# Kernel tuning notes

Measured on AMD Instinct MI355X. Metric: run time of the kernel, lower is better.

## Reference

```python
import jax, jax.numpy as jnp
import numpy as np

SIZE = 1024
CODE_DIM = 256
N = 65536

def setup_inputs() -> dict:
    key = jax.random.key(0)
    k1, k2 = jax.random.split(key)
    z = jax.random.normal(k1, (N, CODE_DIM), dtype=jnp.float32)
    # nn.Embedding weight initialized uniform(-1/size, 1/size)
    weight = jax.random.uniform(k2, (SIZE, CODE_DIM), dtype=jnp.float32,
                                minval=-1.0 / SIZE, maxval=1.0 / SIZE)
    return {"z": z, "weight": weight}

def reference(z, weight):
    flat = z.reshape(-1, CODE_DIM)                       # [N, D]
    distances = (jnp.sum(flat ** 2, axis=1, keepdims=True)
                 - 2.0 * flat @ weight.T
                 + jnp.sum(weight ** 2, axis=1)[None, :])  # [N, SIZE]
    encoding_indices = jnp.argmax(-distances, axis=1)     # [N]
    quantized = weight[encoding_indices]                  # [N, D]
    return quantized, encoding_indices
```

## Files before the change

### kernel.cpp

```cpp
#include <hip/hip_runtime.h>
#include <hip/hip_bf16.h>
#include <stdint.h>
#include <float.h>


constexpr int NROWS = 65536;
constexpr int D     = 256;
constexpr int CODES = 1024;

constexpr float TAU_SCREEN = 2.5e-4f;
constexpr int   MAXPAIRS   = 7000000;

typedef __attribute__((ext_vector_type(8))) short short8;
typedef __attribute__((ext_vector_type(4))) float f32x4;

__device__ __forceinline__ void gl2lds16(const unsigned short* g, unsigned short* l) {
    __builtin_amdgcn_global_load_lds(
        (const __attribute__((address_space(1))) void*)g,
        (__attribute__((address_space(3))) void*)l, 16, 0, 0);
}

__device__ __forceinline__ unsigned short f2bf(float x) {
    union { __hip_bfloat16 h; unsigned short u; } c;
    c.h = __float2bfloat16(x);
    return c.u;
}

__device__ __forceinline__ uint4 pack8(float4 a, float4 b) {
    union { unsigned short u[8]; uint4 v; } p;
    p.u[0] = f2bf(a.x); p.u[1] = f2bf(a.y); p.u[2] = f2bf(a.z); p.u[3] = f2bf(a.w);
    p.u[4] = f2bf(b.x); p.u[5] = f2bf(b.y); p.u[6] = f2bf(b.z); p.u[7] = f2bf(b.w);
    return p.v;
}

__device__ __forceinline__ void cvt8(const float* __restrict__ src,
                                     unsigned short* __restrict__ dst, int i) {
    const float4* s = (const float4*)src + (size_t)i * 2;
    *(uint4*)(dst + (size_t)i * 8) = pack8(s[0], s[1]);
}

__global__ __launch_bounds__(256) void vq_prep(const float* __restrict__ w,
                                               unsigned short* __restrict__ wbf,
                                               float* __restrict__ Cn,
                                               int* __restrict__ cnt,
                                               int* __restrict__ pcnt,
                                               unsigned long long* __restrict__ packed) {
    const int b = blockIdx.x;
    const int t = threadIdx.x;
    if (b < 128) {
        cvt8(w, wbf, b * 256 + t);
    } else if (b < 132) {
        const int row = (b - 128) * 256 + t;
        const float4* p = (const float4*)(w + (size_t)row * D);
        float res[2];
        #pragma unroll
        for (int h = 0; h < 2; ++h) {
            float r[8];
            #pragma unroll
            for (int j = 0; j < 8; ++j) r[j] = 0.f;
            #pragma unroll 4
            for (int mm = 0; mm < 16; ++mm) {
                const float4 v0 = p[h * 32 + mm * 2];
                const float4 v1 = p[h * 32 + mm * 2 + 1];
                r[0] = __fadd_rn(r[0], __fmul_rn(v0.x, v0.x));
                r[1] = __fadd_rn(r[1], __fmul_rn(v0.y, v0.y));
                r[2] = __fadd_rn(r[2], __fmul_rn(v0.z, v0.z));
                r[3] = __fadd_rn(r[3], __fmul_rn(v0.w, v0.w));
                r[4] = __fadd_rn(r[4], __fmul_rn(v1.x, v1.x));
                r[5] = __fadd_rn(r[5], __fmul_rn(v1.y, v1.y));
                r[6] = __fadd_rn(r[6], __fmul_rn(v1.z, v1.z));
                r[7] = __fadd_rn(r[7], __fmul_rn(v1.w, v1.w));
            }
            res[h] = __fadd_rn(__fadd_rn(__fadd_rn(r[0], r[1]), __fadd_rn(r[2], r[3])),
                               __fadd_rn(__fadd_rn(r[4], r[5]), __fadd_rn(r[6], r[7])));
        }
        Cn[row] = __fadd_rn(res[0], res[1]);
    } else {
        const int i = (b - 132) * 256 + t;
        packed[i] = ~0ull;
        if (i == 0) { *cnt = 0; *pcnt = 0; }
    }
}

__global__ __launch_bounds__(512) void vq_screen(const float* __restrict__ z,
                                                 const unsigned short* __restrict__ wbf,
                                                 const float* __restrict__ Cn,
                                                 int* __restrict__ idx_out,
                                                 int* __restrict__ flagged,
                                                 int* __restrict__ cnt,
                                                 float* __restrict__ m1_out) {
    __shared__ unsigned short zT[128 * 256];
    __shared__ unsigned short wT[2][128 * 64];
    __shared__ float Cs[1024];
    __shared__ float rm1s[2][128];
    __shared__ float rm2s[2][128];
    __shared__ int   ris[2][128];

    const int t    = threadIdx.x;
    const int wv   = t >> 6;
    const int l    = t & 63;
    const int wm   = wv >> 1;
    const int wn   = wv & 1;
    const int m    = l & 15;
    const int quad = l >> 4;
    const int row0 = blockIdx.x * 128;

    const int  srow8   = l >> 3;
    const int  schunk  = (l & 7) ^ srow8;
    const size_t laneoff = (size_t)srow8 * D + schunk * 8;

    #pragma unroll
    for (int i = 0; i < 8; ++i) {
        const int flat = i * 512 + t;
        const int r    = flat >> 5;
        const int gch  = flat & 31;
        const float4* src = (const float4*)(z + (size_t)(row0 + r) * D + gch * 8);
        *(uint4*)&zT[r * 256 + ((gch ^ (r & 7)) * 8)] = pack8(src[0], src[1]);
    }
    for (int i = t; i < 1024; i += 512) Cs[i] = Cn[i];

    float m1[2][4], m2[2][4];
    int   bi[2][4];
    f32x4 acc[2][4];
    #pragma unroll
    for (int mi = 0; mi < 2; ++mi)
        #pragma unroll
        for (int r = 0; r < 4; ++r) {
            m1[mi][r] = FLT_MAX; m2[mi][r] = FLT_MAX; bi[mi][r] = 0;
            acc[mi][r] = (f32x4){0.f, 0.f, 0.f, 0.f};
        }

    #define STAGE(s_, buf_) do {                                                    \
        const int nb_ = (s_) >> 2, ks_ = (s_) & 3;                                  \
        _Pragma("unroll")                                                           \
        for (int i_ = 0; i_ < 2; ++i_) {                                            \
            const int u_ = wv * 2 + i_;                                             \
            gl2lds16(wbf + (size_t)(nb_ * 128 + u_ * 8) * D + ks_ * 64 + laneoff,   \
                     &wT[buf_][u_ * 512]);                                          \
        }                                                                           \
    } while (0)

    STAGE(0, 0);
    __syncthreads();

    #pragma unroll 2
    for (int s = 0; s < 32; ++s) {
        const int cur = s & 1;
        if (s < 31) {
            STAGE(s + 1, cur ^ 1);
            asm volatile("s_waitcnt vmcnt(2) lgkmcnt(0)" ::: "memory");
        } else {
            asm volatile("s_waitcnt vmcnt(0) lgkmcnt(0)" ::: "memory");
        }
        asm volatile("s_barrier" ::: "memory");

        #pragma unroll
        for (int kk = 0; kk < 2; ++kk) {
            short8 a[2], b[4];
            const int ch   = kk * 4 + quad;
            const int gchA = (s & 3) * 8 + ch;
            const int coB  = (ch ^ (m & 7)) * 8;
            #pragma unroll
            for (int mi = 0; mi < 2; ++mi)
                a[mi] = *(const short8*)&zT[(wm * 32 + mi * 16 + m) * 256
                                            + ((gchA ^ (m & 7)) * 8)];
            #pragma unroll
            for (int ni = 0; ni < 4; ++ni)
                b[ni] = *(const short8*)&wT[cur][(wn * 64 + ni * 16 + m) * 64 + coB];
            #pragma unroll
            for (int mi = 0; mi < 2; ++mi)
                #pragma unroll
                for (int ni = 0; ni < 4; ++ni)
                    acc[mi][ni] = __builtin_amdgcn_mfma_f32_16x16x32_bf16(
                        a[mi], b[ni], acc[mi][ni], 0, 0, 0);
        }
        asm volatile("s_barrier" ::: "memory");

        if ((s & 3) == 3) {
            const int nb = s >> 2;
            #pragma unroll
            for (int ni = 0; ni < 4; ++ni) {
                const int code = nb * 128 + wn * 64 + ni * 16 + m;
                const float c  = Cs[code];
                #pragma unroll
                for (int mi = 0; mi < 2; ++mi)
                    #pragma unroll
                    for (int r = 0; r < 4; ++r) {
                        const float v  = fmaf(-2.0f, acc[mi][ni][r], c);
                        const float o1 = m1[mi][r];
                        bi[mi][r] = (v < o1) ? code : bi[mi][r];
                        m2[mi][r] = __builtin_amdgcn_fmed3f(o1, m2[mi][r], v);
                        m1[mi][r] = fminf(o1, v);
                        acc[mi][ni][r] = 0.f;
                    }
            }
        }
    }
    #undef STAGE

    #pragma unroll
    for (int mi = 0; mi < 2; ++mi)
        #pragma unroll
        for (int r = 0; r < 4; ++r) {
            float a1 = m1[mi][r], a2 = m2[mi][r];
            int   ai = bi[mi][r];
            #pragma unroll
            for (int off = 1; off <= 8; off <<= 1) {
                const float o1 = __shfl_xor(a1, off, 64);
                const float o2 = __shfl_xor(a2, off, 64);
                const int   oi = __shfl_xor(ai, off, 64);
                const float n1 = fminf(a1, o1);
                const float n2 = fminf(fminf(a2, o2), fmaxf(a1, o1));
                ai = (o1 < a1) ? oi : ai;
                a1 = n1; a2 = n2;
            }
            m1[mi][r] = a1; m2[mi][r] = a2; bi[mi][r] = ai;
        }

    if (m == 0) {
        #pragma unroll
        for (int mi = 0; mi < 2; ++mi)
            #pragma unroll
            for (int r = 0; r < 4; ++r) {
                const int rl = wm * 32 + mi * 16 + quad * 4 + r;
                rm1s[wn][rl] = m1[mi][r];
                rm2s[wn][rl] = m2[mi][r];
                ris[wn][rl]  = bi[mi][r];
            }
    }
    __syncthreads();
    if (t < 128) {
        float a1 = rm1s[0][t], a2 = rm2s[0][t];
        int   ai = ris[0][t];
        const float o1 = rm1s[1][t], o2 = rm2s[1][t];
        const int   oi = ris[1][t];
        const float n1 = fminf(a1, o1);
        const float n2 = fminf(fminf(a2, o2), fmaxf(a1, o1));
        ai = (o1 < a1) ? oi : ai;
        a1 = n1; a2 = n2;
        const int row = row0 + t;
        idx_out[row] = ai;
        m1_out[row]  = a1;
        if (a2 - a1 < TAU_SCREEN) {
            int p = atomicAdd(cnt, 1);
            flagged[p] = row;
        }
    }
}

__global__ __launch_bounds__(256) void vq_cand(const float* __restrict__ z,
                                               const unsigned short* __restrict__ wbf,
                                               const float* __restrict__ Cn,
                                               const float* __restrict__ m1g,
                                               const int* __restrict__ flagged,
                                               const int* __restrict__ cnt,
                                               uint32_t* __restrict__ pairs,
                                               int* __restrict__ pcnt) {
    __shared__ union SM {
        struct { unsigned short zT[128 * 256]; unsigned short wT[2][128 * 64]; } tl;
        uint32_t list[16384];
    } sm;
    __shared__ int rows_s[128];
    __shared__ int lcnt;
    __shared__ int gbase;

    const int t    = threadIdx.x;
    const int wv   = t >> 6;
    const int l    = t & 63;
    const int wm   = wv >> 1;
    const int wn   = wv & 1;
    const int m    = l & 15;
    const int quad = l >> 4;

    const int  srow8   = l >> 3;
    const int  schunk  = (l & 7) ^ srow8;
    const size_t laneoff_w = (size_t)srow8 * D + schunk * 8;

    const int n     = *cnt;
    const int njobs = ((n + 127) >> 7) << 3;

    for (int job = blockIdx.x; job < njobs; job += gridDim.x) {
        const int tile = job >> 3;
        const int nb   = job & 7;
        __syncthreads();
        if (t < 128) {
            const int fi = tile * 128 + t;
            rows_s[t] = (fi < n) ? flagged[fi] : -1;
        }
        if (t == 0) lcnt = 0;
        __syncthreads();

        #pragma unroll
        for (int i = 0; i < 16; ++i) {
            const int flat = i * 256 + t;
            const int r    = flat >> 5;
            const int gch  = flat & 31;
            const int rr   = rows_s[r] < 0 ? 0 : rows_s[r];
            const float4* src = (const float4*)(z + (size_t)rr * D + gch * 8);
            *(uint4*)&sm.tl.zT[r * 256 + ((gch ^ (r & 7)) * 8)] = pack8(src[0], src[1]);
        }

        int   rowid[4][4];
        float thr[4][4];
        #pragma unroll
        for (int mi = 0; mi < 4; ++mi)
            #pragma unroll
            for (int r = 0; r < 4; ++r) {
                const int rl = wm * 64 + mi * 16 + quad * 4 + r;
                const int ri = rows_s[rl];
                rowid[mi][r] = ri;
                thr[mi][r]   = (ri >= 0) ? m1g[ri] + TAU_SCREEN : -FLT_MAX;
            }

        f32x4 acc[4][4];
        #pragma unroll
        for (int mi = 0; mi < 4; ++mi)
            #pragma unroll
            for (int ni = 0; ni < 4; ++ni) acc[mi][ni] = (f32x4){0.f, 0.f, 0.f, 0.f};

        #define STAGEC(ks_, buf_) do {                                                \
            _Pragma("unroll")                                                         \
            for (int i_ = 0; i_ < 4; ++i_) {                                          \
                const int u_ = wv * 4 + i_;                                           \
                gl2lds16(wbf + (size_t)(nb * 128 + u_ * 8) * D + (ks_) * 64           \
                             + laneoff_w,                                             \
                         &sm.tl.wT[buf_][u_ * 512]);                                  \
            }                                                                         \
        } while (0)

        STAGEC(0, 0);
        __syncthreads();

        for (int ks = 0; ks < 4; ++ks) {
            const int cur = ks & 1;
            if (ks < 3) {
                STAGEC(ks + 1, cur ^ 1);
                asm volatile("s_waitcnt vmcnt(4) lgkmcnt(0)" ::: "memory");
            } else {
                asm volatile("s_waitcnt vmcnt(0) lgkmcnt(0)" ::: "memory");
            }
            asm volatile("s_barrier" ::: "memory");
            #pragma unroll
            for (int kk = 0; kk < 2; ++kk) {
                short8 a[4], b[4];
                const int ch   = kk * 4 + quad;
                const int gchA = ks * 8 + ch;
                const int coB  = (ch ^ (m & 7)) * 8;
                #pragma unroll
                for (int mi = 0; mi < 4; ++mi)
                    a[mi] = *(const short8*)&sm.tl.zT[(wm * 64 + mi * 16 + m) * 256
                                                      + ((gchA ^ (m & 7)) * 8)];
                #pragma unroll
                for (int ni = 0; ni < 4; ++ni)
                    b[ni] = *(const short8*)&sm.tl.wT[cur][(wn * 64 + ni * 16 + m) * 64 + coB];
                #pragma unroll
                for (int mi = 0; mi < 4; ++mi)
                    #pragma unroll
                    for (int ni = 0; ni < 4; ++ni)
                        acc[mi][ni] = __builtin_amdgcn_mfma_f32_16x16x32_bf16(
                            a[mi], b[ni], acc[mi][ni], 0, 0, 0);
            }
            asm volatile("s_barrier" ::: "memory");
        }
        #undef STAGEC

        #pragma unroll
        for (int ni = 0; ni < 4; ++ni) {
            const int code = nb * 128 + wn * 64 + ni * 16 + m;
            const float c  = Cn[code];
            #pragma unroll
            for (int mi = 0; mi < 4; ++mi)
                #pragma unroll
                for (int r = 0; r < 4; ++r) {
                    const float v = fmaf(-2.0f, acc[mi][ni][r], c);
                    if (v < thr[mi][r]) {
                        const int p = atomicAdd(&lcnt, 1);
                        sm.list[p] = ((uint32_t)rowid[mi][r] << 16) | (uint32_t)code;
                    }
                }
        }
        __syncthreads();
        if (t == 0) gbase = atomicAdd(pcnt, lcnt);
        __syncthreads();
        const int nc = lcnt;
        const int gb = gbase;
        for (int i = t; i < nc; i += 256) {
            const int p = gb + i;
            if (p < MAXPAIRS) pairs[p] = sm.list[i];
        }
    }
}

__global__ __launch_bounds__(256) void vq_exact(const float* __restrict__ z,
                                                const float* __restrict__ w,
                                                const float* __restrict__ Cn,
                                                const uint32_t* __restrict__ pairs,
                                                const int* __restrict__ pcnt,
                                                unsigned long long* __restrict__ packed) {
    const int np0 = *pcnt;
    const int np  = np0 < MAXPAIRS ? np0 : MAXPAIRS;
    for (int g = blockIdx.x * 256 + threadIdx.x; g < np; g += gridDim.x * 256) {
        const uint32_t pr = pairs[g];
        const int row  = (int)(pr >> 16);
        const int code = (int)(pr & 0xffffu);
        const float4* zp = (const float4*)(z + (size_t)row * D);
        const float4* wp = (const float4*)(w + (size_t)code * D);
        float B = 0.f;
        float res[2];
        #pragma unroll
        for (int b = 0; b < 2; ++b) {
            float r[8];
            #pragma unroll
            for (int j = 0; j < 8; ++j) r[j] = 0.f;
            #pragma unroll 4
            for (int mm = 0; mm < 16; ++mm) {
                const float4 z0 = zp[b * 32 + mm * 2];
                const float4 z1 = zp[b * 32 + mm * 2 + 1];
                const float4 w0 = wp[b * 32 + mm * 2];
                const float4 w1 = wp[b * 32 + mm * 2 + 1];
                r[0] = __fadd_rn(r[0], __fmul_rn(z0.x, z0.x));
                r[1] = __fadd_rn(r[1], __fmul_rn(z0.y, z0.y));
                r[2] = __fadd_rn(r[2], __fmul_rn(z0.z, z0.z));
                r[3] = __fadd_rn(r[3], __fmul_rn(z0.w, z0.w));
                r[4] = __fadd_rn(r[4], __fmul_rn(z1.x, z1.x));
                r[5] = __fadd_rn(r[5], __fmul_rn(z1.y, z1.y));
                r[6] = __fadd_rn(r[6], __fmul_rn(z1.z, z1.z));
                r[7] = __fadd_rn(r[7], __fmul_rn(z1.w, z1.w));
                B = fmaf(z0.x, w0.x, B); B = fmaf(z0.y, w0.y, B);
                B = fmaf(z0.z, w0.z, B); B = fmaf(z0.w, w0.w, B);
                B = fmaf(z1.x, w1.x, B); B = fmaf(z1.y, w1.y, B);
                B = fmaf(z1.z, w1.z, B); B = fmaf(z1.w, w1.w, B);
            }
            res[b] = __fadd_rn(__fadd_rn(__fadd_rn(r[0], r[1]), __fadd_rn(r[2], r[3])),
                               __fadd_rn(__fadd_rn(r[4], r[5]), __fadd_rn(r[6], r[7])));
        }
        const float A = __fadd_rn(res[0], res[1]);
        const float d = __fadd_rn(__fsub_rn(A, __fmul_rn(2.0f, B)), Cn[code]);
        const uint32_t bits = __float_as_uint(d);
        const uint32_t ord  = (bits & 0x80000000u) ? ~bits : (bits | 0x80000000u);
        const unsigned long long key =
            ((unsigned long long)ord << 32) | (unsigned long long)(uint32_t)code;
        atomicMin(&packed[row], key);
    }
}

__global__ __launch_bounds__(256) void vq_unpack(const int* __restrict__ flagged,
                                                 const int* __restrict__ cnt,
                                                 const unsigned long long* __restrict__ packed,
                                                 int* __restrict__ idx) {
    const int n = *cnt;
    for (int g = blockIdx.x * 256 + threadIdx.x; g < n; g += gridDim.x * 256) {
        const int row = flagged[g];
        idx[row] = (int)(packed[row] & 0xffffffffull);
    }
}

__global__ __launch_bounds__(256) void vq_gather(const float* __restrict__ w,
                                                 const int* __restrict__ idx,
                                                 float* __restrict__ outq,
                                                 float* __restrict__ outi) {
    const int t    = threadIdx.x;
    const int lane = t & 63;
    const int sub  = t >> 6;
    const int row0 = blockIdx.x * 128;
    #pragma unroll 4
    for (int it = 0; it < 32; ++it) {
        const int row = row0 + it * 4 + sub;
        const int j   = idx[row];
        ((float4*)outq)[(size_t)row * 64 + lane] = ((const float4*)w)[(size_t)j * 64 + lane];
        if (lane == 0) outi[row] = (float)j;
    }
}

extern "C" void kernel_launch(void* const* d_in, const int* in_sizes, int n_in,
                              void* d_out, int out_size, void* d_ws, size_t ws_size,
                              hipStream_t stream) {
    const float* z = (const float*)d_in[0];
    const float* w = (const float*)d_in[1];
    float* outq = (float*)d_out;
    float* outi = outq + (size_t)NROWS * D;

    unsigned short*     wbf    = (unsigned short*)((char*)d_out + 33554432);
    float*              Cn     = (float*)((char*)d_out + 34078720);
    float*              m1g    = (float*)((char*)d_out + 36700160);
    unsigned long long* packed = (unsigned long long*)((char*)d_out + 37224448);
    uint32_t*           pairs  = (uint32_t*)((char*)d_out + 37748736);

    char* ws      = (char*)d_ws;
    int*  idx     = (int*)ws;
    int*  flagged = (int*)(ws + 262144);
    int*  cnt     = (int*)(ws + 524288);
    int*  pcnt    = (int*)(ws + 524292);

    vq_prep<<<388, 256, 0, stream>>>(w, wbf, Cn, cnt, pcnt, packed);
    vq_screen<<<NROWS / 128, 512, 0, stream>>>(z, wbf, Cn, idx, flagged, cnt, m1g);
    vq_cand<<<512, 256, 0, stream>>>(z, wbf, Cn, m1g, flagged, cnt, pairs, pcnt);
    vq_exact<<<256, 256, 0, stream>>>(z, w, Cn, pairs, pcnt, packed);
    vq_unpack<<<64, 256, 0, stream>>>(flagged, cnt, packed, idx);
    vq_gather<<<NROWS / 128, 256, 0, stream>>>(w, idx, outq, outi);
}
```

Before: 224.6 us.

## Keep z tile in registers and alias its LDS with codebook buffers

Each wave now loads its whole bf16 slice of the z tile from LDS into registers once, before the main loop. The z staging area is then reused for the double-buffered codebook tiles through a union, which cuts LDS per block so more blocks can fit on a CU. The launch bounds add a minimum-occupancy hint. The register array is indexed with a runtime-dependent index (s&3), and the tighter register budget may force scratch spills or select chains, which could cancel the gain from fewer LDS reads.

Result: slower. 273.2 us (+21.6%).

```diff
diff --git a/kernel.cpp b/kernel.cpp
--- a/kernel.cpp
+++ b/kernel.cpp
@@ -82,15 +82,17 @@
     }
 }
 
-__global__ __launch_bounds__(512) void vq_screen(const float* __restrict__ z,
-                                                 const unsigned short* __restrict__ wbf,
-                                                 const float* __restrict__ Cn,
-                                                 int* __restrict__ idx_out,
-                                                 int* __restrict__ flagged,
-                                                 int* __restrict__ cnt,
-                                                 float* __restrict__ m1_out) {
-    __shared__ unsigned short zT[128 * 256];
-    __shared__ unsigned short wT[2][128 * 64];
+__global__ __launch_bounds__(512, 4) void vq_screen(const float* __restrict__ z,
+                                                    const unsigned short* __restrict__ wbf,
+                                                    const float* __restrict__ Cn,
+                                                    int* __restrict__ idx_out,
+                                                    int* __restrict__ flagged,
+                                                    int* __restrict__ cnt,
+                                                    float* __restrict__ m1_out) {
+    __shared__ union USM {
+        unsigned short zT[128 * 256];
+        unsigned short wT[2][128 * 64];
+    } u;
     __shared__ float Cs[1024];
     __shared__ float rm1s[2][128];
     __shared__ float rm2s[2][128];
@@ -115,9 +117,23 @@
         const int r    = flat >> 5;
         const int gch  = flat & 31;
         const float4* src = (const float4*)(z + (size_t)(row0 + r) * D + gch * 8);
-        *(uint4*)&zT[r * 256 + ((gch ^ (r & 7)) * 8)] = pack8(src[0], src[1]);
+        *(uint4*)&u.zT[r * 256 + ((gch ^ (r & 7)) * 8)] = pack8(src[0], src[1]);
     }
     for (int i = t; i < 1024; i += 512) Cs[i] = Cn[i];
+    __syncthreads();
+
+    short8 areg[2][8];
+    #pragma unroll
+    for (int mi = 0; mi < 2; ++mi)
+        #pragma unroll
+        for (int ks = 0; ks < 4; ++ks)
+            #pragma unroll
+            for (int kk = 0; kk < 2; ++kk) {
+                const int gch = ks * 8 + kk * 4 + quad;
+                areg[mi][ks * 2 + kk] = *(const short8*)
+                    &u.zT[(wm * 32 + mi * 16 + m) * 256 + ((gch ^ (m & 7)) * 8)];
+            }
+    __syncthreads();
 
     float m1[2][4], m2[2][4];
     int   bi[2][4];
@@ -136,7 +152,7 @@
         for (int i_ = 0; i_ < 2; ++i_) {                                            \
             const int u_ = wv * 2 + i_;                                             \
             gl2lds16(wbf + (size_t)(nb_ * 128 + u_ * 8) * D + ks_ * 64 + laneoff,   \
-                     &wT[buf_][u_ * 512]);                                          \
+                     &u.wT[buf_][u_ * 512]);                                        \
         }                                                                           \
     } while (0)
 
@@ -156,23 +172,19 @@
 
         #pragma unroll
         for (int kk = 0; kk < 2; ++kk) {
-            short8 a[2], b[4];
-            const int ch   = kk * 4 + quad;
-            const int gchA = (s & 3) * 8 + ch;
-            const int coB  = (ch ^ (m & 7)) * 8;
-            #pragma unroll
-            for (int mi = 0; mi < 2; ++mi)
-                a[mi] = *(const short8*)&zT[(wm * 32 + mi * 16 + m) * 256
-                                            + ((gchA ^ (m & 7)) * 8)];
+            short8 b[4];
+            const int ch  = kk * 4 + quad;
+            const int coB = (ch ^ (m & 7)) * 8;
             #pragma unroll
             for (int ni = 0; ni < 4; ++ni)
-                b[ni] = *(const short8*)&wT[cur][(wn * 64 + ni * 16 + m) * 64 + coB];
+                b[ni] = *(const short8*)&u.wT[cur][(wn * 64 + ni * 16 + m) * 64 + coB];
+            const int ai = (s & 3) * 2 + kk;
             #pragma unroll
             for (int mi = 0; mi < 2; ++mi)
                 #pragma unroll
                 for (int ni = 0; ni < 4; ++ni)
                     acc[mi][ni] = __builtin_amdgcn_mfma_f32_16x16x32_bf16(
-                        a[mi], b[ni], acc[mi][ni], 0, 0, 0);
+                        areg[mi][ai], b[ni], acc[mi][ni], 0, 0, 0);
         }
         asm volatile("s_barrier" ::: "memory");
 
```
